# Kernel tuning notes

Hardware: AMD Instinct MI355X
Metric: run time of the kernel (lower is better)

## Reference

```python
import jax, jax.numpy as jnp
import numpy as np

NUM_HEADS = 8
LN_EPS = 1e-5


def _ln(x, g, b):
    mu = x.mean(-1, keepdims=True)
    xc = x - mu
    v = (xc * xc).mean(-1, keepdims=True)
    return xc * jax.lax.rsqrt(v + LN_EPS) * g + b


def setup_inputs() -> dict:
    key = jax.random.key(0)
    B, T, D, NI, NT = 16, 512, 256, 85, 77
    L, FF, TH = 2, 1024, 32
    ks = iter(jax.random.split(key, 40))
    def nrm(shape, std):
        return jax.random.normal(next(ks), shape, jnp.float32) * std
    inp = {
        'img_tokens': nrm((B, NI, D), 1.0),
        'text_tokens': nrm((B, NT, D), 1.0),
        'task_tokens': nrm((T, D), 0.02),
        'type_task': nrm((D,), 0.02),
        'type_img': nrm((D,), 0.02),
        'type_txt': nrm((D,), 0.02),
        'in_ln_g': jnp.ones((D,), jnp.float32), 'in_ln_b': jnp.zeros((D,), jnp.float32),
        'Wqkv': nrm((L, 3 * D, D), 1.0 / np.sqrt(D)), 'bqkv': jnp.zeros((L, 3 * D), jnp.float32),
        'Wo': nrm((L, D, D), 1.0 / np.sqrt(D)), 'bo': jnp.zeros((L, D), jnp.float32),
        'ln1_g': jnp.ones((L, D), jnp.float32), 'ln1_b': jnp.zeros((L, D), jnp.float32),
        'ln2_g': jnp.ones((L, D), jnp.float32), 'ln2_b': jnp.zeros((L, D), jnp.float32),
        'W1': nrm((L, FF, D), 1.0 / np.sqrt(D)), 'b1': jnp.zeros((L, FF), jnp.float32),
        'W2': nrm((L, D, FF), 1.0 / np.sqrt(FF)), 'b2': jnp.zeros((L, D), jnp.float32),
        'out_ln_g': jnp.ones((D,), jnp.float32), 'out_ln_b': jnp.zeros((D,), jnp.float32),
        'tw1': nrm((T, TH, D), 1.0 / np.sqrt(D)), 'tb1': jnp.zeros((T, TH), jnp.float32),
        'tw2': nrm((T, TH), 1.0 / np.sqrt(TH)), 'tb2': jnp.zeros((T,), jnp.float32),
        'text_mask': jnp.arange(NT)[None, :] < jax.random.randint(next(ks), (B, 1), 10, NT + 1),
        'labels': jax.random.randint(next(ks), (B, T), -1, 2),
    }
    return inp


def reference(img_tokens, text_tokens, task_tokens, type_task, type_img, type_txt,
              in_ln_g, in_ln_b, Wqkv, bqkv, Wo, bo, ln1_g, ln1_b, ln2_g, ln2_b,
              W1, b1, W2, b2, out_ln_g, out_ln_b, tw1, tb1, tw2, tb2,
              text_mask, labels):
    B, NI, D = img_tokens.shape
    T = task_tokens.shape[0]
    L = Wqkv.shape[0]
    hd = D // NUM_HEADS
    available = labels != -1                                   # (B, T)
    n_avail = available.sum(axis=1)                            # (B,)
    # Route B: stable-sort available task ids to the front (permutation per row)
    order = jnp.argsort((~available).astype(jnp.int32), axis=1, stable=True)  # (B, T)
    task_toks = task_tokens[order] + type_task                 # (B, T, D)
    seq = jnp.concatenate([task_toks, img_tokens + type_img, text_tokens + type_txt], axis=1)
    seq = _ln(seq, in_ln_g, in_ln_b)
    task_pad = jnp.arange(T)[None, :] >= n_avail[:, None]
    pad = jnp.concatenate([task_pad, jnp.zeros((B, NI), bool), ~text_mask], axis=1)
    bias = jnp.where(pad, -1e9, 0.0).astype(seq.dtype)[:, None, None, :]  # key-padding mask
    scale = 1.0 / np.sqrt(hd)
    S = seq.shape[1]
    for l in range(L):  # pre-LN transformer encoder layers (eval mode)
        h = _ln(seq, ln1_g[l], ln1_b[l])
        qkv = h @ Wqkv[l].T + bqkv[l]
        q, k, v = jnp.split(qkv, 3, axis=-1)
        q = q.reshape(B, S, NUM_HEADS, hd)
        k = k.reshape(B, S, NUM_HEADS, hd)
        v = v.reshape(B, S, NUM_HEADS, hd)
        scores = jnp.einsum('bqhd,bkhd->bhqk', q, k) * scale + bias
        attn = jax.nn.softmax(scores, axis=-1)
        o = jnp.einsum('bhqk,bkhd->bqhd', attn, v).reshape(B, S, D)
        seq = seq + o @ Wo[l].T + bo[l]
        h2 = _ln(seq, ln2_g[l], ln2_b[l])
        seq = seq + jax.nn.gelu(h2 @ W1[l].T + b1[l], approximate=False) @ W2[l].T + b2[l]
    task_out = _ln(seq[:, :T], out_ln_g, out_ln_b)             # (B, T, D)
    # undo the per-row permutation so task t's token sits at column t, then
    # apply all per-task towers as one grouped matmul (MoE dispatch/combine)
    y = jnp.zeros_like(task_out).at[jnp.arange(B)[:, None], order].set(task_out)
    hsz = jax.nn.relu(jnp.einsum('btd,thd->bth', y, tw1) + tb1[None])
    out = jnp.einsum('bth,th->bt', hsz, tw2) + tb2[None]
    return jnp.where(available, out, jnp.zeros((), out.dtype))
```

## Files before the change

kernel.cpp:

```cpp
#include <hip/hip_runtime.h>
#include <hip/hip_bf16.h>
#include <math.h>

constexpr int B_  = 16;
constexpr int T_  = 512;
constexpr int D_  = 256;
constexpr int NI_ = 85;
constexpr int NT_ = 77;
constexpr int S_  = T_ + NI_ + NT_;
constexpr int M_  = B_ * S_;
constexpr int FF_ = 1024;
constexpr int TH_ = 32;
constexpr int NH_ = 8;
constexpr int KT_ = 704;

constexpr float MASK_NEG = -30000.0f;

constexpr int N_FT = 26;
constexpr int OFF_[N_FT + 1] = {
    0,
    348160,
    663552,
    794624,
    794880,
    795136,
    795392,
    795648,
    795904,
    1189120,
    1190656,
    1321728,
    1322240,
    1322752,
    1323264,
    1323776,
    1324288,
    1848576,
    1850624,
    2374912,
    2375424,
    2375680,
    2375936,
    6570240,
    6586624,
    6603008,
    6603520
};
constexpr int TOTAL_ELEMS = OFF_[N_FT];

typedef __attribute__((ext_vector_type(8))) short bfrag;
typedef __attribute__((ext_vector_type(4))) float f32x4;

__device__ inline float bf2f(__hip_bfloat16 x) { return __bfloat162float(x); }
__device__ inline __hip_bfloat16 f2bf(float x) { return __float2bfloat16(x); }
__device__ inline float bfbits2f(unsigned short u) {
    unsigned int x = ((unsigned int)u) << 16;
    float f;
    __builtin_memcpy(&f, &x, 4);
    return f;
}
__device__ inline float wsum64(float v) {
    #pragma unroll
    for (int m = 32; m >= 1; m >>= 1) v += __shfl_xor(v, m, 64);
    return v;
}
__device__ inline bool is_f32_mode(const void* ln_g_raw) {
    return (*(const unsigned int*)ln_g_raw) == 0x3F800000u;
}

__device__ inline void gload_lds16(const __hip_bfloat16* g, __hip_bfloat16* l) {
#if defined(__has_builtin) && __has_builtin(__builtin_amdgcn_global_load_lds)
    __builtin_amdgcn_global_load_lds(
        (const __attribute__((address_space(1))) unsigned int*)g,
        (__attribute__((address_space(3))) unsigned int*)l, 16, 0, 0);
#else
    *reinterpret_cast<uint4*>(l) = *reinterpret_cast<const uint4*>(g);
#endif
}

struct Ptrs { const void* p[N_FT]; };

__global__ __launch_bounds__(256) void k_convert(Ptrs ptrs, __hip_bfloat16* __restrict__ canon) {
    int idx = blockIdx.x * 256 + threadIdx.x;
    if (idx >= TOTAL_ELEMS) return;
    bool f32 = is_f32_mode(ptrs.p[6]);
    int t = 0;
    #pragma unroll
    for (int i = 1; i < N_FT; i++) if (idx >= OFF_[i]) t = i;
    int local = idx - OFF_[t];
    if (f32) canon[idx] = f2bf(((const float*)ptrs.p[t])[local]);
    else     canon[idx] = ((const __hip_bfloat16*)ptrs.p[t])[local];
}

__global__ void k_prep(const int* __restrict__ labels, int* __restrict__ inv,
                       int* __restrict__ n_avail) {
    __shared__ int sc[T_];
    int b = blockIdx.x, t = threadIdx.x;
    int av = (labels[b * T_ + t] != -1) ? 1 : 0;
    sc[t] = av;
    __syncthreads();
    for (int off = 1; off < T_; off <<= 1) {
        int v = sc[t];
        int u = (t >= off) ? sc[t - off] : 0;
        __syncthreads();
        sc[t] = v + u;
        __syncthreads();
    }
    int incl  = sc[t];
    int excl  = incl - av;
    int total = sc[T_ - 1];
    inv[b * T_ + t] = av ? excl : (total + (t - excl));
    if (t == 0) n_avail[b] = total;
}

__global__ void k_build(const __hip_bfloat16* __restrict__ img,
                        const __hip_bfloat16* __restrict__ txt,
                        const __hip_bfloat16* __restrict__ task,
                        const __hip_bfloat16* __restrict__ ty_task,
                        const __hip_bfloat16* __restrict__ ty_img,
                        const __hip_bfloat16* __restrict__ ty_txt,
                        const __hip_bfloat16* __restrict__ g,
                        const __hip_bfloat16* __restrict__ bln,
                        const void* __restrict__ text_mask,
                        const int* __restrict__ inv,
                        const int* __restrict__ n_avail,
                        float* __restrict__ seq,
                        float* __restrict__ bias) {
    int blk = blockIdx.x;
    int b = blk / S_, j = blk % S_;
    int lane = threadIdx.x;

    int dest;
    float bias_v;
    const __hip_bfloat16* src;
    const __hip_bfloat16* tvec;
    if (j < T_) {
        dest = inv[b * T_ + j];
        src = task + (size_t)j * D_;
        tvec = ty_task;
        bias_v = (dest >= n_avail[b]) ? MASK_NEG : 0.f;
    } else if (j < T_ + NI_) {
        dest = j;
        src = img + (size_t)(b * NI_ + (j - T_)) * D_;
        tvec = ty_img;
        bias_v = 0.f;
    } else {
        int x2 = j - T_ - NI_;
        dest = j;
        src = txt + (size_t)(b * NT_ + x2) * D_;
        tvec = ty_txt;
        const unsigned char* mb = (const unsigned char*)text_mask;
        bool is_byte = (mb[1] != 0);
        int mv = is_byte ? (int)mb[b * NT_ + x2]
                         : ((const int*)text_mask)[b * NT_ + x2];
        bias_v = mv ? 0.f : MASK_NEG;
    }

    float x[4];
    float s = 0.f, ss = 0.f;
    #pragma unroll
    for (int i = 0; i < 4; i++) {
        int d = lane * 4 + i;
        x[i] = bf2f(src[d]) + bf2f(tvec[d]);
        s += x[i];
        ss += x[i] * x[i];
    }
    s = wsum64(s);
    ss = wsum64(ss);
    float mean = s * (1.f / D_);
    float var  = ss * (1.f / D_) - mean * mean;
    float r    = rsqrtf(fmaxf(var, 0.f) + 1e-5f);

    float* orow = seq + ((size_t)b * S_ + dest) * D_;
    #pragma unroll
    for (int i = 0; i < 4; i++) {
        int d = lane * 4 + i;
        orow[d] = (x[i] - mean) * r * bf2f(g[d]) + bf2f(bln[d]);
    }
    if (lane == 0) bias[b * S_ + dest] = bias_v;
}

__global__ void k_ln(const float* __restrict__ x,
                     const __hip_bfloat16* __restrict__ g,
                     const __hip_bfloat16* __restrict__ bb,
                     __hip_bfloat16* __restrict__ y, int nrows) {
    int w = threadIdx.x >> 6, lane = threadIdx.x & 63;
    int row = blockIdx.x * 4 + w;
    if (row >= nrows) return;
    const float* xr = x + (size_t)row * D_;
    float4 vv = *reinterpret_cast<const float4*>(xr + lane * 4);
    float v[4] = {vv.x, vv.y, vv.z, vv.w};
    float s = v[0] + v[1] + v[2] + v[3];
    float ss = v[0]*v[0] + v[1]*v[1] + v[2]*v[2] + v[3]*v[3];
    s = wsum64(s);
    ss = wsum64(ss);
    float mean = s * (1.f / D_);
    float var  = ss * (1.f / D_) - mean * mean;
    float r    = rsqrtf(fmaxf(var, 0.f) + 1e-5f);
    __hip_bfloat16 tmp[4];
    #pragma unroll
    for (int i = 0; i < 4; i++) {
        int d = lane * 4 + i;
        tmp[i] = f2bf((v[i] - mean) * r * bf2f(g[d]) + bf2f(bb[d]));
    }
    *reinterpret_cast<uint2*>(y + (size_t)row * D_ + lane * 4) = *reinterpret_cast<uint2*>(tmp);
}

template <int GELU, int RESF>
__global__ __launch_bounds__(256) void k_gemm(const __hip_bfloat16* __restrict__ A,
                                              const __hip_bfloat16* __restrict__ W,
                                              const __hip_bfloat16* __restrict__ bias,
                                              const float* __restrict__ res,
                                              void* __restrict__ Cout,
                                              int Mm, int N, int K) {
    constexpr int STAGE_BYTES = 64 * 32 * 2 * 2;
    constexpr int EPI_BYTES   = RESF ? (64 * 68 * 4) : (64 * 72 * 2);
    constexpr int SH_BYTES    = (STAGE_BYTES > EPI_BYTES) ? STAGE_BYTES : EPI_BYTES;
    __shared__ __align__(16) unsigned char Sh[SH_BYTES];
    __hip_bfloat16* As = (__hip_bfloat16*)Sh;
    __hip_bfloat16* Ws = (__hip_bfloat16*)(Sh + 4096);
    unsigned char*  Es = Sh;

    int m0 = blockIdx.x * 64;
    int n0 = blockIdx.y * 64;
    int tid = threadIdx.x;
    int w = tid >> 6, lane = tid & 63;
    int lrow = lane & 15, quad = lane >> 4;

    f32x4 acc[4] = {};

    int r = tid >> 2;
    int kq = (tid & 3) * 8;
    int gmr = min(m0 + r, Mm - 1);
    const __hip_bfloat16* Ar = A + (size_t)gmr * K + kq;
    const __hip_bfloat16* Wr = W + (size_t)(n0 + r) * K + kq;
    __hip_bfloat16* Al = &As[r * 32 + kq];
    __hip_bfloat16* Wl = &Ws[r * 32 + kq];

    for (int k0 = 0; k0 < K; k0 += 32) {
        __syncthreads();
        gload_lds16(Ar + k0, Al);
        gload_lds16(Wr + k0, Wl);
        __syncthreads();

        bfrag af = *reinterpret_cast<const bfrag*>(&As[(w * 16 + lrow) * 32 + quad * 8]);
        #pragma unroll
        for (int nt = 0; nt < 4; nt++) {
            bfrag bf = *reinterpret_cast<const bfrag*>(&Ws[(nt * 16 + lrow) * 32 + quad * 8]);
            acc[nt] = __builtin_amdgcn_mfma_f32_16x16x32_bf16(af, bf, acc[nt], 0, 0, 0);
        }
    }
    __syncthreads();

    #pragma unroll
    for (int nt = 0; nt < 4; nt++) {
        int col = nt * 16 + lrow;
        float bv = bf2f(bias[n0 + col]);
        #pragma unroll
        for (int rg = 0; rg < 4; rg++) {
            int row = w * 16 + quad * 4 + rg;
            float v = acc[nt][rg] + bv;
            if (GELU) v = 0.5f * v * (1.f + erff(v * 0.70710678118654752f));
            if (RESF) ((float*)Es)[row * 68 + col] = v;
            else      ((__hip_bfloat16*)Es)[row * 72 + col] = f2bf(v);
        }
    }
    __syncthreads();

    if (RESF) {
        #pragma unroll
        for (int i = 0; i < 4; i++) {
            int c = tid + i * 256;
            int row = c >> 4, off = (c & 15) * 4;
            int gm = m0 + row;
            if (gm < Mm) {
                const float* src = &((const float*)Es)[row * 68 + off];
                float4 v4 = make_float4(src[0], src[1], src[2], src[3]);
                const float4 r4 = *reinterpret_cast<const float4*>(&res[(size_t)gm * N + n0 + off]);
                v4.x += r4.x; v4.y += r4.y; v4.z += r4.z; v4.w += r4.w;
                *reinterpret_cast<float4*>(&((float*)Cout)[(size_t)gm * N + n0 + off]) = v4;
            }
        }
    } else {
        #pragma unroll
        for (int i = 0; i < 2; i++) {
            int c = tid + i * 256;
            int row = c >> 3, off = (c & 7) * 8;
            int gm = m0 + row;
            if (gm < Mm) {
                uint4 v4 = *reinterpret_cast<const uint4*>(&((const __hip_bfloat16*)Es)[row * 72 + off]);
                *reinterpret_cast<uint4*>(&((__hip_bfloat16*)Cout)[(size_t)gm * N + n0 + off]) = v4;
            }
        }
    }
}

__global__ __launch_bounds__(256) void k_fattn(const __hip_bfloat16* __restrict__ qkv,
                                               const float* __restrict__ bias,
                                               __hip_bfloat16* __restrict__ out) {
    __shared__ __align__(16) __hip_bfloat16 Vt[2][32 * 72];
    __shared__ __align__(16) __hip_bfloat16 Ps[4][16 * 72];
    __shared__ float Bs[KT_];
    int b = blockIdx.z, h = blockIdx.y;
    int tid = threadIdx.x;
    int wave = tid >> 6, lane = tid & 63;
    int lrow = lane & 15, quad = lane >> 4;
    int q0 = blockIdx.x * 64 + wave * 16;

    const float scale = 0.17677669529663687f;
    const __hip_bfloat16* base = qkv + (size_t)b * S_ * 768;
    const float* brow = bias + b * S_;

    for (int i = tid; i < KT_; i += 256) Bs[i] = (i < S_) ? brow[i] : MASK_NEG;

    int qr = q0 + lrow; if (qr >= S_) qr = S_ - 1;
    bfrag qf = *reinterpret_cast<const bfrag*>(base + (size_t)qr * 768 + h * 32 + quad * 8);

    float m[4] = {-3e38f, -3e38f, -3e38f, -3e38f};
    float l[4] = {0.f, 0.f, 0.f, 0.f};
    f32x4 O[2] = {};

    int skey = lane;
    int sd   = wave * 8;

    const int ktiles = KT_ / 64;

    bfrag kf_cur[4], vv_cur;
    #pragma unroll
    for (int nt = 0; nt < 4; nt++) {
        int kr = min(nt * 16 + lrow, S_ - 1);
        kf_cur[nt] = *reinterpret_cast<const bfrag*>(base + (size_t)kr * 768 + 256 + h * 32 + quad * 8);
    }
    {
        int kr = min(skey, S_ - 1);
        vv_cur = *reinterpret_cast<const bfrag*>(base + (size_t)kr * 768 + 512 + h * 32 + sd);
    }

    for (int t = 0; t < ktiles; t++) {
        int k0 = t * 64;
        __hip_bfloat16* vb = Vt[t & 1];

        #pragma unroll
        for (int i = 0; i < 8; i++) vb[(sd + i) * 72 + skey] = ((const __hip_bfloat16*)&vv_cur)[i];
        __syncthreads();

        bfrag kf_nxt[4], vv_nxt;
        {
            int kb = k0 + 64;
            #pragma unroll
            for (int nt = 0; nt < 4; nt++) {
                int kr = min(kb + nt * 16 + lrow, S_ - 1);
                kf_nxt[nt] = *reinterpret_cast<const bfrag*>(base + (size_t)kr * 768 + 256 + h * 32 + quad * 8);
            }
            int kr = min(kb + skey, S_ - 1);
            vv_nxt = *reinterpret_cast<const bfrag*>(base + (size_t)kr * 768 + 512 + h * 32 + sd);
        }

        f32x4 sc4[4];
        #pragma unroll
        for (int nt = 0; nt < 4; nt++) {
            f32x4 z = {};
            sc4[nt] = __builtin_amdgcn_mfma_f32_16x16x32_bf16(qf, kf_cur[nt], z, 0, 0, 0);
            float bv = Bs[k0 + nt * 16 + lrow];
            #pragma unroll
            for (int rg = 0; rg < 4; rg++) sc4[nt][rg] = sc4[nt][rg] * scale + bv;
        }

        float alpha[4];
        #pragma unroll
        for (int rg = 0; rg < 4; rg++) {
            float rm = fmaxf(fmaxf(sc4[0][rg], sc4[1][rg]), fmaxf(sc4[2][rg], sc4[3][rg]));
            #pragma unroll
            for (int mm2 = 1; mm2 <= 8; mm2 <<= 1) rm = fmaxf(rm, __shfl_xor(rm, mm2, 64));
            float mn = fmaxf(m[rg], rm);
            alpha[rg] = __expf(m[rg] - mn);
            m[rg] = mn;
            float rs = 0.f;
            #pragma unroll
            for (int nt = 0; nt < 4; nt++) {
                float pv = __expf(sc4[nt][rg] - mn);
                sc4[nt][rg] = pv;
                rs += pv;
            }
            #pragma unroll
            for (int mm2 = 1; mm2 <= 8; mm2 <<= 1) rs += __shfl_xor(rs, mm2, 64);
            l[rg] = l[rg] * alpha[rg] + rs;
        }
        #pragma unroll
        for (int dt = 0; dt < 2; dt++)
            #pragma unroll
            for (int rg = 0; rg < 4; rg++) O[dt][rg] *= alpha[rg];

        #pragma unroll
        for (int nt = 0; nt < 4; nt++)
            #pragma unroll
            for (int rg = 0; rg < 4; rg++)
                Ps[wave][(quad * 4 + rg) * 72 + nt * 16 + lrow] = f2bf(sc4[nt][rg]);

        bfrag ap0 = *reinterpret_cast<const bfrag*>(&Ps[wave][lrow * 72 + quad * 8]);
        bfrag ap1 = *reinterpret_cast<const bfrag*>(&Ps[wave][lrow * 72 + 32 + quad * 8]);
        #pragma unroll
        for (int dt = 0; dt < 2; dt++) {
            bfrag bv0 = *reinterpret_cast<const bfrag*>(&vb[(dt * 16 + lrow) * 72 + quad * 8]);
            bfrag bv1 = *reinterpret_cast<const bfrag*>(&vb[(dt * 16 + lrow) * 72 + 32 + quad * 8]);
            O[dt] = __builtin_amdgcn_mfma_f32_16x16x32_bf16(ap0, bv0, O[dt], 0, 0, 0);
            O[dt] = __builtin_amdgcn_mfma_f32_16x16x32_bf16(ap1, bv1, O[dt], 0, 0, 0);
        }

        #pragma unroll
        for (int nt = 0; nt < 4; nt++) kf_cur[nt] = kf_nxt[nt];
        vv_cur = vv_nxt;
    }

    #pragma unroll
    for (int rg = 0; rg < 4; rg++) {
        int qrow = q0 + quad * 4 + rg;
        if (qrow < S_) {
            float invl = 1.f / l[rg];
            #pragma unroll
            for (int dt = 0; dt < 2; dt++)
                out[((size_t)b * S_ + qrow) * D_ + h * 32 + dt * 16 + lrow] = f2bf(O[dt][rg] * invl);
        }
    }
}

__global__ __launch_bounds__(256) void k_final(const float* __restrict__ seq,
                                               const int* __restrict__ inv,
                                               const int* __restrict__ labels,
                                               const __hip_bfloat16* __restrict__ g,
                                               const __hip_bfloat16* __restrict__ bb,
                                               const __hip_bfloat16* __restrict__ tw1,
                                               const __hip_bfloat16* __restrict__ tb1,
                                               const __hip_bfloat16* __restrict__ tw2,
                                               const __hip_bfloat16* __restrict__ tb2,
                                               const void* __restrict__ ln_g_raw,
                                               void* __restrict__ out) {
    int idx = blockIdx.x;
    int t = idx >> 4, b = idx & 15;
    int tid = threadIdx.x;
    bool f32o = is_f32_mode(ln_g_raw);

    int lab = labels[b * T_ + t];
    if (lab == -1) {
        if (tid == 0) {
            if (f32o) ((float*)out)[b * T_ + t] = 0.f;
            else      ((__hip_bfloat16*)out)[b * T_ + t] = f2bf(0.f);
        }
        return;
    }

    __shared__ float y[D_];
    __shared__ float hb[TH_];
    __shared__ float rs[4], rq[4];

    int row = inv[b * T_ + t];
    float x = seq[((size_t)b * S_ + row) * D_ + tid];
    float s1 = wsum64(x);
    float s2 = wsum64(x * x);
    int w = tid >> 6, lane = tid & 63;
    if (lane == 0) { rs[w] = s1; rq[w] = s2; }
    __syncthreads();
    float fs = rs[0] + rs[1] + rs[2] + rs[3];
    float fq = rq[0] + rq[1] + rq[2] + rq[3];
    float mean = fs * (1.f / D_);
    float var  = fq * (1.f / D_) - mean * mean;
    float r    = rsqrtf(fmaxf(var, 0.f) + 1e-5f);
    y[tid] = (x - mean) * r * bf2f(g[tid]) + bf2f(bb[tid]);
    __syncthreads();

    int hh = tid >> 3, part = tid & 7;
    const uint4* w4 = reinterpret_cast<const uint4*>(tw1 + ((size_t)t * TH_ + hh) * D_ + part * 32);
    float acc = 0.f;
    #pragma unroll
    for (int i = 0; i < 4; i++) {
        uint4 kv = w4[i];
        unsigned int wd[4] = {kv.x, kv.y, kv.z, kv.w};
        #pragma unroll
        for (int j2 = 0; j2 < 4; j2++) {
            acc += y[part * 32 + i * 8 + j2 * 2]     * bfbits2f((unsigned short)(wd[j2] & 0xffffu));
            acc += y[part * 32 + i * 8 + j2 * 2 + 1] * bfbits2f((unsigned short)(wd[j2] >> 16));
        }
    }
    #pragma unroll
    for (int mm = 4; mm >= 1; mm >>= 1) acc += __shfl_down(acc, mm, 8);
    if (part == 0) {
        float hz = acc + bf2f(tb1[t * TH_ + hh]);
        hz = fmaxf(hz, 0.f);
        hb[hh] = hz * bf2f(tw2[t * TH_ + hh]);
    }
    __syncthreads();
    if (tid == 0) {
        float o = bf2f(tb2[t]);
        #pragma unroll
        for (int i = 0; i < TH_; i++) o += hb[i];
        if (f32o) ((float*)out)[b * T_ + t] = o;
        else      ((__hip_bfloat16*)out)[b * T_ + t] = f2bf(o);
    }
}

extern "C" void kernel_launch(void* const* d_in, const int* in_sizes, int n_in,
                              void* d_out, int out_size, void* d_ws, size_t ws_size,
                              hipStream_t stream) {
    const void* tmask  = d_in[26];
    const int*  labels = (const int*)d_in[27];

    char* p = (char*)d_ws;
    auto alloc = [&](size_t bytes) {
        char* r = p;
        p += (bytes + 255) & ~size_t(255);
        return r;
    };
    __hip_bfloat16* canon  = (__hip_bfloat16*)alloc(sizeof(__hip_bfloat16) * (size_t)TOTAL_ELEMS);
    int*            inv     = (int*)alloc(sizeof(int) * B_ * T_);
    int*            n_avail = (int*)alloc(sizeof(int) * B_);
    float*          bias    = (float*)alloc(sizeof(float) * M_);
    float*          seqF    = (float*)alloc(sizeof(float) * (size_t)M_ * D_);
    __hip_bfloat16* bufA    = (__hip_bfloat16*)alloc(sizeof(__hip_bfloat16) * (size_t)M_ * D_);
    __hip_bfloat16* bufBig  = (__hip_bfloat16*)alloc(sizeof(__hip_bfloat16) * (size_t)M_ * FF_);

    Ptrs ptrs;
    for (int i = 0; i < N_FT; i++) ptrs.p[i] = d_in[i];
    hipLaunchKernelGGL(k_convert, dim3((TOTAL_ELEMS + 255) / 256), dim3(256), 0, stream,
                       ptrs, canon);

    const __hip_bfloat16* img      = canon + OFF_[0];
    const __hip_bfloat16* txt      = canon + OFF_[1];
    const __hip_bfloat16* task     = canon + OFF_[2];
    const __hip_bfloat16* ty_task  = canon + OFF_[3];
    const __hip_bfloat16* ty_img   = canon + OFF_[4];
    const __hip_bfloat16* ty_txt   = canon + OFF_[5];
    const __hip_bfloat16* in_ln_g  = canon + OFF_[6];
    const __hip_bfloat16* in_ln_b  = canon + OFF_[7];
    const __hip_bfloat16* Wqkv     = canon + OFF_[8];
    const __hip_bfloat16* bqkv     = canon + OFF_[9];
    const __hip_bfloat16* Wo       = canon + OFF_[10];
    const __hip_bfloat16* bo       = canon + OFF_[11];
    const __hip_bfloat16* ln1_g    = canon + OFF_[12];
    const __hip_bfloat16* ln1_b    = canon + OFF_[13];
    const __hip_bfloat16* ln2_g    = canon + OFF_[14];
    const __hip_bfloat16* ln2_b    = canon + OFF_[15];
    const __hip_bfloat16* W1       = canon + OFF_[16];
    const __hip_bfloat16* b1       = canon + OFF_[17];
    const __hip_bfloat16* W2       = canon + OFF_[18];
    const __hip_bfloat16* b2       = canon + OFF_[19];
    const __hip_bfloat16* out_ln_g = canon + OFF_[20];
    const __hip_bfloat16* out_ln_b = canon + OFF_[21];
    const __hip_bfloat16* tw1      = canon + OFF_[22];
    const __hip_bfloat16* tb1      = canon + OFF_[23];
    const __hip_bfloat16* tw2      = canon + OFF_[24];
    const __hip_bfloat16* tb2      = canon + OFF_[25];

    hipLaunchKernelGGL(k_prep, dim3(B_), dim3(T_), 0, stream, labels, inv, n_avail);
    hipLaunchKernelGGL(k_build, dim3(B_ * S_), dim3(64), 0, stream,
                       img, txt, task, ty_task, ty_img, ty_txt, in_ln_g, in_ln_b,
                       tmask, inv, n_avail, seqF, bias);

    const int mtiles = (M_ + 63) / 64;
    const int ln_blocks = (M_ + 3) / 4;
    const int qtiles = (S_ + 63) / 64;

    for (int l = 0; l < 2; l++) {
        hipLaunchKernelGGL(k_ln, dim3(ln_blocks), dim3(256), 0, stream,
                           seqF, ln1_g + l * D_, ln1_b + l * D_, bufA, M_);
        hipLaunchKernelGGL((k_gemm<0, 0>), dim3(mtiles, 12), dim3(256), 0, stream,
                           bufA, Wqkv + (size_t)l * 3 * D_ * D_, bqkv + l * 3 * D_,
                           (const float*)nullptr, (void*)bufBig, M_, 3 * D_, D_);
        hipLaunchKernelGGL(k_fattn, dim3(qtiles, NH_, B_), dim3(256), 0, stream,
                           bufBig, bias, bufA);
        hipLaunchKernelGGL((k_gemm<0, 1>), dim3(mtiles, 4), dim3(256), 0, stream,
                           bufA, Wo + (size_t)l * D_ * D_, bo + l * D_, seqF,
                           (void*)seqF, M_, D_, D_);
        hipLaunchKernelGGL(k_ln, dim3(ln_blocks), dim3(256), 0, stream,
                           seqF, ln2_g + l * D_, ln2_b + l * D_, bufA, M_);
        hipLaunchKernelGGL((k_gemm<1, 0>), dim3(mtiles, 16), dim3(256), 0, stream,
                           bufA, W1 + (size_t)l * FF_ * D_, b1 + l * FF_,
                           (const float*)nullptr, (void*)bufBig, M_, FF_, D_);
        hipLaunchKernelGGL((k_gemm<0, 1>), dim3(mtiles, 4), dim3(256), 0, stream,
                           bufBig, W2 + (size_t)l * D_ * FF_, b2 + l * D_, seqF,
                           (void*)seqF, M_, D_, FF_);
    }

    hipLaunchKernelGGL(k_final, dim3(T_ * B_), dim3(256), 0, stream,
                       seqF, inv, labels, out_ln_g, out_ln_b,
                       tw1, tb1, tw2, tb2, d_in[6], d_out);
}
```

Before: 427.7 us.

## Fuse LayerNorms into residual GEMM epilogues with full-row tiles

After: 436.7 us. 1.02x slower.

```diff
diff --git a/kernel.cpp b/kernel.cpp
--- a/kernel.cpp
+++ b/kernel.cpp
@@ -121,10 +121,13 @@
                         const __hip_bfloat16* __restrict__ ty_txt,
                         const __hip_bfloat16* __restrict__ g,
                         const __hip_bfloat16* __restrict__ bln,
+                        const __hip_bfloat16* __restrict__ g1,
+                        const __hip_bfloat16* __restrict__ b1,
                         const void* __restrict__ text_mask,
                         const int* __restrict__ inv,
                         const int* __restrict__ n_avail,
                         float* __restrict__ seq,
+                        __hip_bfloat16* __restrict__ h1,
                         float* __restrict__ bias) {
     int blk = blockIdx.x;
     int b = blk / S_, j = blk % S_;
@@ -171,55 +174,44 @@
     float var  = ss * (1.f / D_) - mean * mean;
     float r    = rsqrtf(fmaxf(var, 0.f) + 1e-5f);
 
+    float y[4];
+    float s2 = 0.f, ss2 = 0.f;
     float* orow = seq + ((size_t)b * S_ + dest) * D_;
     #pragma unroll
     for (int i = 0; i < 4; i++) {
         int d = lane * 4 + i;
-        orow[d] = (x[i] - mean) * r * bf2f(g[d]) + bf2f(bln[d]);
-    }
-    if (lane == 0) bias[b * S_ + dest] = bias_v;
-}
-
-__global__ void k_ln(const float* __restrict__ x,
-                     const __hip_bfloat16* __restrict__ g,
-                     const __hip_bfloat16* __restrict__ bb,
-                     __hip_bfloat16* __restrict__ y, int nrows) {
-    int w = threadIdx.x >> 6, lane = threadIdx.x & 63;
-    int row = blockIdx.x * 4 + w;
-    if (row >= nrows) return;
-    const float* xr = x + (size_t)row * D_;
-    float4 vv = *reinterpret_cast<const float4*>(xr + lane * 4);
-    float v[4] = {vv.x, vv.y, vv.z, vv.w};
-    float s = v[0] + v[1] + v[2] + v[3];
-    float ss = v[0]*v[0] + v[1]*v[1] + v[2]*v[2] + v[3]*v[3];
-    s = wsum64(s);
-    ss = wsum64(ss);
-    float mean = s * (1.f / D_);
-    float var  = ss * (1.f / D_) - mean * mean;
-    float r    = rsqrtf(fmaxf(var, 0.f) + 1e-5f);
+        y[i] = (x[i] - mean) * r * bf2f(g[d]) + bf2f(bln[d]);
+        orow[d] = y[i];
+        s2 += y[i];
+        ss2 += y[i] * y[i];
+    }
+    s2 = wsum64(s2);
+    ss2 = wsum64(ss2);
+    float mean2 = s2 * (1.f / D_);
+    float var2  = ss2 * (1.f / D_) - mean2 * mean2;
+    float r2    = rsqrtf(fmaxf(var2, 0.f) + 1e-5f);
     __hip_bfloat16 tmp[4];
     #pragma unroll
     for (int i = 0; i < 4; i++) {
         int d = lane * 4 + i;
-        tmp[i] = f2bf((v[i] - mean) * r * bf2f(g[d]) + bf2f(bb[d]));
-    }
-    *reinterpret_cast<uint2*>(y + (size_t)row * D_ + lane * 4) = *reinterpret_cast<uint2*>(tmp);
-}
-
-template <int GELU, int RESF>
+        tmp[i] = f2bf((y[i] - mean2) * r2 * bf2f(g1[d]) + bf2f(b1[d]));
+    }
+    *reinterpret_cast<uint2*>(h1 + ((size_t)b * S_ + dest) * D_ + lane * 4) =
+        *reinterpret_cast<uint2*>(tmp);
+    if (lane == 0) bias[b * S_ + dest] = bias_v;
+}
+
+template <int GELU>
 __global__ __launch_bounds__(256) void k_gemm(const __hip_bfloat16* __restrict__ A,
                                               const __hip_bfloat16* __restrict__ W,
                                               const __hip_bfloat16* __restrict__ bias,
-                                              const float* __restrict__ res,
-                                              void* __restrict__ Cout,
+                                              __hip_bfloat16* __restrict__ Cout,
                                               int Mm, int N, int K) {
-    constexpr int STAGE_BYTES = 64 * 32 * 2 * 2;
-    constexpr int EPI_BYTES   = RESF ? (64 * 68 * 4) : (64 * 72 * 2);
-    constexpr int SH_BYTES    = (STAGE_BYTES > EPI_BYTES) ? STAGE_BYTES : EPI_BYTES;
+    constexpr int SH_BYTES = 64 * 72 * 2;
     __shared__ __align__(16) unsigned char Sh[SH_BYTES];
     __hip_bfloat16* As = (__hip_bfloat16*)Sh;
     __hip_bfloat16* Ws = (__hip_bfloat16*)(Sh + 4096);
-    unsigned char*  Es = Sh;
+    __hip_bfloat16* Es = (__hip_bfloat16*)Sh;
 
     int m0 = blockIdx.x * 64;
     int n0 = blockIdx.y * 64;
@@ -261,37 +253,129 @@
             int row = w * 16 + quad * 4 + rg;
             float v = acc[nt][rg] + bv;
             if (GELU) v = 0.5f * v * (1.f + erff(v * 0.70710678118654752f));
-            if (RESF) ((float*)Es)[row * 68 + col] = v;
-            else      ((__hip_bfloat16*)Es)[row * 72 + col] = f2bf(v);
-        }
-    }
-    __syncthreads();
-
-    if (RESF) {
-        #pragma unroll
-        for (int i = 0; i < 4; i++) {
-            int c = tid + i * 256;
-            int row = c >> 4, off = (c & 15) * 4;
-            int gm = m0 + row;
-            if (gm < Mm) {
-                const float* src = &((const float*)Es)[row * 68 + off];
-                float4 v4 = make_float4(src[0], src[1], src[2], src[3]);
-                const float4 r4 = *reinterpret_cast<const float4*>(&res[(size_t)gm * N + n0 + off]);
-                v4.x += r4.x; v4.y += r4.y; v4.z += r4.z; v4.w += r4.w;
-                *reinterpret_cast<float4*>(&((float*)Cout)[(size_t)gm * N + n0 + off]) = v4;
-            }
-        }
-    } else {
-        #pragma unroll
-        for (int i = 0; i < 2; i++) {
-            int c = tid + i * 256;
-            int row = c >> 3, off = (c & 7) * 8;
-            int gm = m0 + row;
-            if (gm < Mm) {
-                uint4 v4 = *reinterpret_cast<const uint4*>(&((const __hip_bfloat16*)Es)[row * 72 + off]);
-                *reinterpret_cast<uint4*>(&((__hip_bfloat16*)Cout)[(size_t)gm * N + n0 + off]) = v4;
-            }
-        }
+            Es[row * 72 + col] = f2bf(v);
+        }
+    }
+    __syncthreads();
+
+    #pragma unroll
+    for (int i = 0; i < 2; i++) {
+        int c = tid + i * 256;
+        int row = c >> 3, off = (c & 7) * 8;
+        int gm = m0 + row;
+        if (gm < Mm) {
+            uint4 v4 = *reinterpret_cast<const uint4*>(&Es[row * 72 + off]);
+            *reinterpret_cast<uint4*>(&Cout[(size_t)gm * N + off + n0]) = v4;
+        }
+    }
+}
+
+template <int LNOUT>
+__global__ __launch_bounds__(256) void k_gemm_lnres(const __hip_bfloat16* __restrict__ A,
+                                                    const __hip_bfloat16* __restrict__ W,
+                                                    const __hip_bfloat16* __restrict__ bias,
+                                                    float* __restrict__ seq,
+                                                    const __hip_bfloat16* __restrict__ lng,
+                                                    const __hip_bfloat16* __restrict__ lnb,
+                                                    __hip_bfloat16* __restrict__ lnout,
+                                                    int K) {
+    constexpr int N = 256;
+    constexpr int ESTRIDE = 260;
+    __shared__ __align__(16) unsigned char Sh[32 * ESTRIDE * 4];
+    __hip_bfloat16* As = (__hip_bfloat16*)Sh;
+    __hip_bfloat16* Ws = (__hip_bfloat16*)(Sh + 2048);
+    float*          Es = (float*)Sh;
+
+    int m0 = blockIdx.x * 32;
+    int tid = threadIdx.x;
+    int w = tid >> 6, lane = tid & 63;
+    int lrow = lane & 15, quad = lane >> 4;
+
+    f32x4 acc[2][4] = {};
+
+    const __hip_bfloat16* Ar = A + (size_t)(m0 + (tid >> 2)) * K + (tid & 3) * 8;
+    __hip_bfloat16* Al = As + tid * 8;
+    const __hip_bfloat16* Wr[4];
+    __hip_bfloat16* Wl[4];
+    #pragma unroll
+    for (int i = 0; i < 4; i++) {
+        int c = tid + i * 256;
+        Wr[i] = W + (size_t)(c >> 2) * K + (c & 3) * 8;
+        Wl[i] = Ws + c * 8;
+    }
+
+    for (int k0 = 0; k0 < K; k0 += 32) {
+        __syncthreads();
+        if (tid < 128) gload_lds16(Ar + k0, Al);
+        #pragma unroll
+        for (int i = 0; i < 4; i++) gload_lds16(Wr[i] + k0, Wl[i]);
+        __syncthreads();
+
+        bfrag af[2], bf[4];
+        #pragma unroll
+        for (int mt = 0; mt < 2; mt++)
+            af[mt] = *reinterpret_cast<const bfrag*>(&As[(mt * 16 + lrow) * 32 + quad * 8]);
+        #pragma unroll
+        for (int nt = 0; nt < 4; nt++)
+            bf[nt] = *reinterpret_cast<const bfrag*>(&Ws[(w * 64 + nt * 16 + lrow) * 32 + quad * 8]);
+        #pragma unroll
+        for (int mt = 0; mt < 2; mt++)
+            #pragma unroll
+            for (int nt = 0; nt < 4; nt++)
+                acc[mt][nt] = __builtin_amdgcn_mfma_f32_16x16x32_bf16(af[mt], bf[nt], acc[mt][nt], 0, 0, 0);
+    }
+    __syncthreads();
+
+    #pragma unroll
+    for (int nt = 0; nt < 4; nt++) {
+        int col = w * 64 + nt * 16 + lrow;
+        float bv = bf2f(bias[col]);
+        #pragma unroll
+        for (int mt = 0; mt < 2; mt++)
+            #pragma unroll
+            for (int rg = 0; rg < 4; rg++)
+                Es[(mt * 16 + quad * 4 + rg) * ESTRIDE + col] = acc[mt][nt][rg] + bv;
+    }
+    __syncthreads();
+
+    int row = tid >> 3, part = tid & 7;
+    size_t gm = (size_t)(m0 + row);
+    float* seqrow = seq + gm * N + part * 32;
+    float t[32];
+    float s = 0.f, ss = 0.f;
+    #pragma unroll
+    for (int j = 0; j < 8; j++) {
+        float4 e = *reinterpret_cast<const float4*>(&Es[row * ESTRIDE + part * 32 + j * 4]);
+        float4 r4 = *reinterpret_cast<const float4*>(&seqrow[j * 4]);
+        float v0 = e.x + r4.x, v1 = e.y + r4.y, v2 = e.z + r4.z, v3 = e.w + r4.w;
+        t[j * 4 + 0] = v0; t[j * 4 + 1] = v1; t[j * 4 + 2] = v2; t[j * 4 + 3] = v3;
+        s += v0 + v1 + v2 + v3;
+        ss += v0 * v0 + v1 * v1 + v2 * v2 + v3 * v3;
+    }
+    #pragma unroll
+    for (int j = 0; j < 8; j++) {
+        float4 o = make_float4(t[j * 4 + 0], t[j * 4 + 1], t[j * 4 + 2], t[j * 4 + 3]);
+        *reinterpret_cast<float4*>(&seqrow[j * 4]) = o;
+    }
+    if (LNOUT) {
+        #pragma unroll
+        for (int mm = 4; mm >= 1; mm >>= 1) {
+            s  += __shfl_xor(s,  mm, 8);
+            ss += __shfl_xor(ss, mm, 8);
+        }
+        float mean = s * (1.f / N);
+        float var  = ss * (1.f / N) - mean * mean;
+        float r    = rsqrtf(fmaxf(var, 0.f) + 1e-5f);
+        __hip_bfloat16 ob[32];
+        #pragma unroll
+        for (int j = 0; j < 32; j++) {
+            int col = part * 32 + j;
+            ob[j] = f2bf((t[j] - mean) * r * bf2f(lng[col]) + bf2f(lnb[col]));
+        }
+        #pragma unroll
+        for (int j = 0; j < 4; j++)
+            *reinterpret_cast<uint4*>(&lnout[gm * N + part * 32 + j * 8]) =
+                *reinterpret_cast<const uint4*>(&ob[j * 8]);
     }
 }
 
@@ -553,31 +637,34 @@
     hipLaunchKernelGGL(k_prep, dim3(B_), dim3(T_), 0, stream, labels, inv, n_avail);
     hipLaunchKernelGGL(k_build, dim3(B_ * S_), dim3(64), 0, stream,
                        img, txt, task, ty_task, ty_img, ty_txt, in_ln_g, in_ln_b,
-                       tmask, inv, n_avail, seqF, bias);
+                       ln1_g, ln1_b, tmask, inv, n_avail, seqF, bufA, bias);
 
     const int mtiles = (M_ + 63) / 64;
-    const int ln_blocks = (M_ + 3) / 4;
+    const int rtiles = M_ / 32;
     const int qtiles = (S_ + 63) / 64;
 
     for (int l = 0; l < 2; l++) {
-        hipLaunchKernelGGL(k_ln, dim3(ln_blocks), dim3(256), 0, stream,
-                           seqF, ln1_g + l * D_, ln1_b + l * D_, bufA, M_);
-        hipLaunchKernelGGL((k_gemm<0, 0>), dim3(mtiles, 12), dim3(256), 0, stream,
+        hipLaunchKernelGGL((k_gemm<0>), dim3(mtiles, 12), dim3(256), 0, stream,
                            bufA, Wqkv + (size_t)l * 3 * D_ * D_, bqkv + l * 3 * D_,
-                           (const float*)nullptr, (void*)bufBig, M_, 3 * D_, D_);
+                           bufBig, M_, 3 * D_, D_);
         hipLaunchKernelGGL(k_fattn, dim3(qtiles, NH_, B_), dim3(256), 0, stream,
                            bufBig, bias, bufA);
-        hipLaunchKernelGGL((k_gemm<0, 1>), dim3(mtiles, 4), dim3(256), 0, stream,
+        hipLaunchKernelGGL((k_gemm_lnres<1>), dim3(rtiles), dim3(256), 0, stream,
                            bufA, Wo + (size_t)l * D_ * D_, bo + l * D_, seqF,
-                           (void*)seqF, M_, D_, D_);
-        hipLaunchKernelGGL(k_ln, dim3(ln_blocks), dim3(256), 0, stream,
-                           seqF, ln2_g + l * D_, ln2_b + l * D_, bufA, M_);
-        hipLaunchKernelGGL((k_gemm<1, 0>), dim3(mtiles, 16), dim3(256), 0, stream,
+                           ln2_g + l * D_, ln2_b + l * D_, bufA, D_);
+        hipLaunchKernelGGL((k_gemm<1>), dim3(mtiles, 16), dim3(256), 0, stream,
                            bufA, W1 + (size_t)l * FF_ * D_, b1 + l * FF_,
-                           (const float*)nullptr, (void*)bufBig, M_, FF_, D_);
-        hipLaunchKernelGGL((k_gemm<0, 1>), dim3(mtiles, 4), dim3(256), 0, stream,
-                           bufBig, W2 + (size_t)l * D_ * FF_, b2 + l * D_, seqF,
-                           (void*)seqF, M_, D_, FF_);
+                           bufBig, M_, FF_, D_);
+        if (l == 0) {
+            hipLaunchKernelGGL((k_gemm_lnres<1>), dim3(rtiles), dim3(256), 0, stream,
+                               bufBig, W2 + (size_t)l * D_ * FF_, b2 + l * D_, seqF,
+                               ln1_g + 1 * D_, ln1_b + 1 * D_, bufA, FF_);
+        } else {
+            hipLaunchKernelGGL((k_gemm_lnres<0>), dim3(rtiles), dim3(256), 0, stream,
+                               bufBig, W2 + (size_t)l * D_ * FF_, b2 + l * D_, seqF,
+                               (const __hip_bfloat16*)nullptr, (const __hip_bfloat16*)nullptr,
+                               (__hip_bfloat16*)nullptr, FF_);
+        }
     }
 
     hipLaunchKernelGGL(k_final, dim3(T_ * B_), dim3(256), 0, stream,
```
